# Optimization experiments

Hardware: AMD Instinct MI355X
Metric: run time of the kernel (lower is better)

The kernel has to match this reference:

```python
import jax, jax.numpy as jnp
import numpy as np

B, M, D = 512, 96, 512
H = 8            # num_heads
DH = D // H      # head dim
NC = 3           # num_clusters
BETA = 5
MEM = 1024       # memory_size
EPS = 1e-8


def _l2norm(x, axis=-1):
    # torch F.cosine_similarity clamps each norm at eps=1e-8
    n = jnp.linalg.norm(x, axis=axis, keepdims=True)
    return x / jnp.maximum(n, EPS)


def _dynamic_clustering(sims):
    # sims: (B, M). Sort descending, split into NC equal groups,
    # per-group mean and (unbiased) std. (dynamic_clustering is not
    # defined in the source repo; this is the assumed implementation.)
    s = -jnp.sort(-sims, axis=1)               # descending
    g = s.reshape(B, NC, M // NC)
    means = g.mean(axis=-1)                    # (B, NC)
    stds = jnp.std(g, axis=-1, ddof=1)         # (B, NC)
    return means, stds


def setup_inputs() -> dict:
    key = jax.random.key(0)
    ks = jax.random.split(key, 6)
    vis_global = jax.random.normal(ks[0], (B, D), dtype=jnp.float32)
    text_features = jax.random.normal(ks[1], (B, M, D), dtype=jnp.float32)
    scale = 1.0 / np.sqrt(D)
    in_proj_w = jax.random.normal(ks[2], (3 * D, D), dtype=jnp.float32) * scale
    in_proj_b = jnp.zeros((3 * D,), dtype=jnp.float32)
    out_proj_w = jax.random.normal(ks[3], (D, D), dtype=jnp.float32) * scale
    out_proj_b = jnp.zeros((D,), dtype=jnp.float32)
    text_memory = jax.random.normal(ks[4], (MEM, D), dtype=jnp.float32)
    tau_p_log = jnp.log(jnp.asarray(0.1, dtype=jnp.float32))
    tau_n_log = jnp.log(jnp.asarray(0.05, dtype=jnp.float32))
    return dict(vis_global=vis_global, text_features=text_features,
                in_proj_w=in_proj_w, in_proj_b=in_proj_b,
                out_proj_w=out_proj_w, out_proj_b=out_proj_b,
                text_memory=text_memory, tau_p_log=tau_p_log, tau_n_log=tau_n_log)


def reference(vis_global, text_features, in_proj_w, in_proj_b,
              out_proj_w, out_proj_b, text_memory, tau_p_log, tau_n_log):
    # --- dynamic clustering over visual-text cosine sims ---
    sims = jnp.einsum('bd,bmd->bm', _l2norm(vis_global), _l2norm(text_features))
    means, stds = _dynamic_clustering(sims)
    cluster_scores = means / (stds + 1e-6)     # (B, NC)

    # --- MultiheadAttention: 1-token query, M-token key/value ---
    wq, wk, wv = in_proj_w[:D], in_proj_w[D:2 * D], in_proj_w[2 * D:]
    bq, bk, bv = in_proj_b[:D], in_proj_b[D:2 * D], in_proj_b[2 * D:]
    q = (vis_global @ wq.T + bq).reshape(B, H, DH)              # (B,H,DH)
    k = (text_features @ wk.T + bk).reshape(B, M, H, DH)        # (B,M,H,DH)
    v = (text_features @ wv.T + bv).reshape(B, M, H, DH)
    attn = jax.nn.softmax(jnp.einsum('bhd,bmhd->bhm', q, k) / np.sqrt(DH), axis=-1)
    ctx = jnp.einsum('bhm,bmhd->bhd', attn, v).reshape(B, D)
    corrected = ctx @ out_proj_w.T + out_proj_b                 # (B, D)

    tau_p = jnp.exp(tau_p_log)
    tau_n = jnp.exp(tau_n_log)
    pos_sim = jnp.sum(_l2norm(vis_global) * _l2norm(corrected), axis=-1)  # (B,)

    # memory-bank scatter (ptr starts at 0) + negatives, all detached
    corr_sg = jax.lax.stop_gradient(corrected)
    mem = text_memory.at[0:B].set(corr_sg)
    all_negs = jnp.concatenate([jnp.roll(corr_sg, 1, axis=0), mem], axis=0)  # (B+MEM, D)

    neg_sims = _l2norm(vis_global) @ _l2norm(all_negs).T        # (B, B+MEM)
    hard_negs, _ = jax.lax.top_k(neg_sims, BETA)                # (B, BETA)

    pos_term = jnp.exp(pos_sim / tau_p)
    neg_terms = jnp.exp(hard_negs / tau_n).sum(axis=1)
    loss = -jnp.mean(jnp.log(pos_term / (pos_term + neg_terms + 1e-8)))
    return loss, corrected, cluster_scores
```

## Files before the change

kernel.cpp:

```cpp
#include <hip/hip_runtime.h>
#include <math.h>

typedef unsigned short u16;
typedef unsigned int u32;
typedef __attribute__((ext_vector_type(8))) short short8;
typedef __attribute__((ext_vector_type(4))) float f32x4;

#define EPS 1e-8f

__device__ inline float bf2f(u16 u) {
    union { u32 i; float f; } v; v.i = ((u32)u) << 16; return v.f;
}
__device__ inline u16 f2bf(float f) {
    union { float f; u32 u; } v; v.f = f;
    u32 r = v.u + 0x7fffu + ((v.u >> 16) & 1u);
    return (u16)(r >> 16);
}
__device__ inline u32 pack2(float a, float b) {
    return (u32)f2bf(a) | ((u32)f2bf(b) << 16);
}
__device__ inline float wave_sum(float v) {
    for (int off = 32; off; off >>= 1) v += __shfl_xor(v, off, 64);
    return v;
}

__global__ __launch_bounds__(256) void prep(const float* __restrict__ vis,
                                            const float* __restrict__ ipw,
                                            const float* __restrict__ opw,
                                            float* __restrict__ vis_n,
                                            u16* __restrict__ vis_nb,
                                            u16* __restrict__ vis_b,
                                            u16* __restrict__ wqb,
                                            u16* __restrict__ wvb,
                                            u16* __restrict__ wob,
                                            float* __restrict__ loss0)
{
    int bid = blockIdx.x;
    if (bid >= 128) {
        int i = ((bid - 128) * 256 + threadIdx.x) * 4;
        const float* src; u16* dst; int j;
        if (i < 262144)      { j = i;          src = ipw + j;          dst = wqb + j; }
        else if (i < 524288) { j = i - 262144; src = ipw + 524288 + j; dst = wvb + j; }
        else                 { j = i - 524288; src = opw + j;          dst = wob + j; }
        float4 v = *(const float4*)src;
        uint2 pk; pk.x = pack2(v.x, v.y); pk.y = pack2(v.z, v.w);
        *(uint2*)dst = pk;
        return;
    }
    if (bid == 0 && threadIdx.x == 0) loss0[0] = 0.0f;
    int wave = threadIdx.x >> 6, lane = threadIdx.x & 63;
    int b = bid * 4 + wave;
    const float* row = vis + b * 512 + lane * 8;
    float4 x0 = *(const float4*)row;
    float4 x1 = *(const float4*)(row + 4);
    uint4 rk;
    rk.x = pack2(x0.x, x0.y); rk.y = pack2(x0.z, x0.w);
    rk.z = pack2(x1.x, x1.y); rk.w = pack2(x1.z, x1.w);
    *(uint4*)(vis_b + b*512 + lane*8) = rk;
    float ss = x0.x*x0.x + x0.y*x0.y + x0.z*x0.z + x0.w*x0.w
             + x1.x*x1.x + x1.y*x1.y + x1.z*x1.z + x1.w*x1.w;
    ss = wave_sum(ss);
    float inv = 1.0f / fmaxf(sqrtf(ss), EPS);
    float4 y0, y1;
    y0.x = x0.x*inv; y0.y = x0.y*inv; y0.z = x0.z*inv; y0.w = x0.w*inv;
    y1.x = x1.x*inv; y1.y = x1.y*inv; y1.z = x1.z*inv; y1.w = x1.w*inv;
    *(float4*)(vis_n + b*512 + lane*8)     = y0;
    *(float4*)(vis_n + b*512 + lane*8 + 4) = y1;
    uint4 pk;
    pk.x = pack2(y0.x, y0.y); pk.y = pack2(y0.z, y0.w);
    pk.z = pack2(y1.x, y1.y); pk.w = pack2(y1.z, y1.w);
    *(uint4*)(vis_nb + b*512 + lane*8) = pk;
}

__global__ __launch_bounds__(256) void gemm64(const u16* __restrict__ A, int lda,
                                              const u16* __restrict__ B,
                                              const float* __restrict__ bias,
                                              float* __restrict__ Cf, int ldc)
{
    __shared__ __align__(16) u16 As[64 * 64];
    __shared__ __align__(16) u16 Bs[64 * 64];
    const int t = threadIdx.x, lane = t & 63, w = t >> 6;
    const int m0 = blockIdx.x * 64, n0 = blockIdx.y * 64;
    const int wm = (w >> 1) * 32, wn = (w & 1) * 32;
    const int l16 = lane & 15, quad = lane >> 4;
    const int srow = t >> 3, scol = (t & 7) * 8;

    f32x4 acc[2][2];
    for (int i = 0; i < 2; i++)
        for (int j = 0; j < 2; j++)
            for (int e = 0; e < 4; e++) acc[i][j][e] = 0.f;

    for (int ko = 0; ko < 512; ko += 64) {
        __syncthreads();
        #pragma unroll
        for (int i = 0; i < 2; i++) {
            int row = i * 32 + srow;
            *(uint4*)&As[row * 64 + scol] = *(const uint4*)&A[(size_t)(m0 + row) * lda + ko + scol];
            *(uint4*)&Bs[row * 64 + scol] = *(const uint4*)&B[(size_t)(n0 + row) * 512 + ko + scol];
        }
        __syncthreads();
        #pragma unroll
        for (int ks = 0; ks < 2; ks++) {
            short8 af[2], bfr[2];
            #pragma unroll
            for (int i = 0; i < 2; i++)
                af[i] = *(const short8*)&As[(wm + i * 16 + l16) * 64 + ks * 32 + quad * 8];
            #pragma unroll
            for (int j = 0; j < 2; j++)
                bfr[j] = *(const short8*)&Bs[(wn + j * 16 + l16) * 64 + ks * 32 + quad * 8];
            #pragma unroll
            for (int i = 0; i < 2; i++)
                #pragma unroll
                for (int j = 0; j < 2; j++)
                    acc[i][j] = __builtin_amdgcn_mfma_f32_16x16x32_bf16(af[i], bfr[j], acc[i][j], 0, 0, 0);
        }
    }
    for (int i = 0; i < 2; i++) {
        int row = m0 + wm + i * 16 + quad * 4;
        for (int j = 0; j < 2; j++) {
            int col = n0 + wn + j * 16 + l16;
            float bv = bias ? bias[col] : 0.f;
            for (int r = 0; r < 4; r++)
                Cf[(size_t)(row + r) * ldc + col] = acc[i][j][r] + bv;
        }
    }
}

__global__ __launch_bounds__(256) void gemm_head(const u16* __restrict__ u_allb,
                                                 const u16* __restrict__ wvb,
                                                 const float* __restrict__ bv,
                                                 u16* __restrict__ ctxb)
{
    const int h = blockIdx.y;
    const u16* A = u_allb + h * 512;
    const u16* B = wvb + (size_t)h * 64 * 512;
    __shared__ __align__(16) u16 As[64 * 64];
    __shared__ __align__(16) u16 Bs[64 * 64];
    const int t = threadIdx.x, lane = t & 63, w = t >> 6;
    const int m0 = blockIdx.x * 64;
    const int wm = (w >> 1) * 32, wn = (w & 1) * 32;
    const int l16 = lane & 15, quad = lane >> 4;
    const int srow = t >> 3, scol = (t & 7) * 8;

    f32x4 acc[2][2];
    for (int i = 0; i < 2; i++)
        for (int j = 0; j < 2; j++)
            for (int e = 0; e < 4; e++) acc[i][j][e] = 0.f;

    for (int ko = 0; ko < 512; ko += 64) {
        __syncthreads();
        #pragma unroll
        for (int i = 0; i < 2; i++) {
            int row = i * 32 + srow;
            *(uint4*)&As[row * 64 + scol] = *(const uint4*)&A[(size_t)(m0 + row) * 4096 + ko + scol];
            *(uint4*)&Bs[row * 64 + scol] = *(const uint4*)&B[(size_t)row * 512 + ko + scol];
        }
        __syncthreads();
        #pragma unroll
        for (int ks = 0; ks < 2; ks++) {
            short8 af[2], bfr[2];
            #pragma unroll
            for (int i = 0; i < 2; i++)
                af[i] = *(const short8*)&As[(wm + i * 16 + l16) * 64 + ks * 32 + quad * 8];
            #pragma unroll
            for (int j = 0; j < 2; j++)
                bfr[j] = *(const short8*)&Bs[(wn + j * 16 + l16) * 64 + ks * 32 + quad * 8];
            #pragma unroll
            for (int i = 0; i < 2; i++)
                #pragma unroll
                for (int j = 0; j < 2; j++)
                    acc[i][j] = __builtin_amdgcn_mfma_f32_16x16x32_bf16(af[i], bfr[j], acc[i][j], 0, 0, 0);
        }
    }
    for (int i = 0; i < 2; i++) {
        int row = m0 + wm + i * 16 + quad * 4;
        for (int j = 0; j < 2; j++) {
            int col = wn + j * 16 + l16;
            float bb = bv[h * 64 + col];
            for (int r = 0; r < 4; r++)
                ctxb[(size_t)(row + r) * 512 + h * 64 + col] = f2bf(acc[i][j][r] + bb);
        }
    }
}

__global__ __launch_bounds__(256) void qk_proj(const float* __restrict__ q,
                                               const float* __restrict__ wk,
                                               float* __restrict__ qk_all)
{
    int bg = blockIdx.x, h = blockIdx.y;
    int t = threadIdx.x;
    int j = blockIdx.z * 256 + t;
    __shared__ float q8[8][64];
    {
        int r = t >> 5;
        int d0 = (t & 31) * 2;
        const float* qp = q + (bg * 8 + r) * 512 + h * 64 + d0;
        q8[r][d0] = qp[0]; q8[r][d0 + 1] = qp[1];
    }
    __syncthreads();
    float acc[8] = {0, 0, 0, 0, 0, 0, 0, 0};
    const float* wrow = wk + (size_t)(h * 64) * 512 + j;
    #pragma unroll 4
    for (int d = 0; d < 64; d++) {
        float ww = wrow[(size_t)d * 512];
        #pragma unroll
        for (int r = 0; r < 8; r++) acc[r] += q8[r][d] * ww;
    }
    #pragma unroll
    for (int r = 0; r < 8; r++)
        qk_all[((size_t)(bg * 8 + r) * 8 + h) * 512 + j] = acc[r];
}

__global__ __launch_bounds__(1024) void fused_attn(const float* __restrict__ tf,
                                                   const float* __restrict__ vis_n,
                                                   const float* __restrict__ qk_all,
                                                   u16* __restrict__ u_allb,
                                                   float* __restrict__ out_cs)
{
    __shared__ __align__(16) u16 Xs[96 * 520];
    __shared__ __align__(16) u16 Qs[16 * 520];
    __shared__ __align__(16) u16 Ps[16 * 104];
    __shared__ float Sc[16 * 100];
    __shared__ float sm_[96], srt[96], linv[8];

    const int b = blockIdx.x;
    const int t = threadIdx.x, w = t >> 6, lane = t & 63;
    const int l16 = lane & 15, quad = lane >> 4;

    const float4* v4 = (const float4*)(vis_n + b * 512 + lane * 8);
    float4 va = v4[0], vb = v4[1];

    if (w < 8) {
        const float4* q4 = (const float4*)(qk_all + ((size_t)b * 8 + w) * 512 + lane * 8);
        float4 a = q4[0], c = q4[1];
        uint4 pk;
        pk.x = pack2(a.x, a.y); pk.y = pack2(a.z, a.w);
        pk.z = pack2(c.x, c.y); pk.w = pack2(c.z, c.w);
        *(uint4*)&Qs[w * 520 + lane * 8] = pk;
    }

    #pragma unroll
    for (int i = 0; i < 3; i++) {
        int m0r = w + i * 32;
        int m1r = m0r + 16;
        const float4* x4a = (const float4*)(tf + ((size_t)b * 96 + m0r) * 512 + lane * 8);
        const float4* x4b = (const float4*)(tf + ((size_t)b * 96 + m1r) * 512 + lane * 8);
        float4 a0 = x4a[0], c0 = x4a[1];
        float4 a1 = x4b[0], c1 = x4b[1];
        float ss0 = a0.x*a0.x + a0.y*a0.y + a0.z*a0.z + a0.w*a0.w
                  + c0.x*c0.x + c0.y*c0.y + c0.z*c0.z + c0.w*c0.w;
        float dt0 = a0.x*va.x + a0.y*va.y + a0.z*va.z + a0.w*va.w
                  + c0.x*vb.x + c0.y*vb.y + c0.z*vb.z + c0.w*vb.w;
        float ss1 = a1.x*a1.x + a1.y*a1.y + a1.z*a1.z + a1.w*a1.w
                  + c1.x*c1.x + c1.y*c1.y + c1.z*c1.z + c1.w*c1.w;
        float dt1 = a1.x*va.x + a1.y*va.y + a1.z*va.z + a1.w*va.w
                  + c1.x*vb.x + c1.y*vb.y + c1.z*vb.z + c1.w*vb.w;
        #pragma unroll
        for (int off = 32; off; off >>= 1) {
            ss0 += __shfl_xor(ss0, off, 64);
            dt0 += __shfl_xor(dt0, off, 64);
            ss1 += __shfl_xor(ss1, off, 64);
            dt1 += __shfl_xor(dt1, off, 64);
        }
        if (lane == 0) {
            sm_[m0r] = dt0 / fmaxf(sqrtf(ss0), EPS);
            sm_[m1r] = dt1 / fmaxf(sqrtf(ss1), EPS);
        }
        uint4 pk0, pk1;
        pk0.x = pack2(a0.x, a0.y); pk0.y = pack2(a0.z, a0.w);
        pk0.z = pack2(c0.x, c0.y); pk0.w = pack2(c0.z, c0.w);
        pk1.x = pack2(a1.x, a1.y); pk1.y = pack2(a1.z, a1.w);
        pk1.z = pack2(c1.x, c1.y); pk1.w = pack2(c1.z, c1.w);
        *(uint4*)&Xs[m0r * 520 + lane * 8] = pk0;
        *(uint4*)&Xs[m1r * 520 + lane * 8] = pk1;
    }
    __syncthreads();

    if (w < 6) {
        f32x4 acc;
        for (int e = 0; e < 4; e++) acc[e] = 0.f;
        #pragma unroll
        for (int ks = 0; ks < 16; ks++) {
            short8 a = *(const short8*)&Xs[(w * 16 + l16) * 520 + ks * 32 + quad * 8];
            short8 q = *(const short8*)&Qs[l16 * 520 + ks * 32 + quad * 8];
            acc = __builtin_amdgcn_mfma_f32_16x16x32_bf16(a, q, acc, 0, 0, 0);
        }
        #pragma unroll
        for (int r = 0; r < 4; r++)
            Sc[l16 * 100 + w * 16 + quad * 4 + r] = acc[r] * 0.125f;
    }
    __syncthreads();

    if (w < 8) {
        float e0 = __expf(Sc[w * 100 + lane]);
        float e1 = (lane < 32) ? __expf(Sc[w * 100 + 64 + lane]) : 0.f;
        float l = wave_sum(e0 + e1);
        Ps[w * 104 + lane] = f2bf(e0);
        if (lane < 32) Ps[w * 104 + 64 + lane] = f2bf(e1);
        if (lane == 0) linv[w] = 1.0f / l;
    }
    if (t < 96) {
        float v = sm_[t]; int r = 0;
        for (int j = 0; j < 96; j++) {
            float u = sm_[j];
            r += (u > v) || (u == v && j < t);
        }
        srt[r] = v;
    }
    __syncthreads();

    #pragma unroll
    for (int jj = 0; jj < 2; jj++) {
        int n0 = (w * 2 + jj) * 16;
        f32x4 acc;
        for (int e = 0; e < 4; e++) acc[e] = 0.f;
        #pragma unroll
        for (int ks = 0; ks < 3; ks++) {
            short8 ap = *(const short8*)&Ps[l16 * 104 + ks * 32 + quad * 8];
            short8 bx;
            #pragma unroll
            for (int j = 0; j < 8; j++)
                bx[j] = (short)Xs[(ks * 32 + quad * 8 + j) * 520 + n0 + l16];
            acc = __builtin_amdgcn_mfma_f32_16x16x32_bf16(ap, bx, acc, 0, 0, 0);
        }
        if (quad < 2) {
            #pragma unroll
            for (int r = 0; r < 4; r++) {
                int h = quad * 4 + r;
                u_allb[((size_t)b * 8 + h) * 512 + n0 + l16] = f2bf(acc[r] * linv[h]);
            }
        }
    }
    if (t < 3) {
        float mean = 0.f;
        #pragma unroll 8
        for (int i = 0; i < 32; i++) mean += srt[t * 32 + i];
        mean *= (1.0f / 32.0f);
        float var = 0.f;
        #pragma unroll 8
        for (int i = 0; i < 32; i++) { float d = srt[t * 32 + i] - mean; var += d * d; }
        var *= (1.0f / 31.0f);
        out_cs[b * 3 + t] = mean / (sqrtf(var) + 1e-6f);
    }
}

__global__ __launch_bounds__(256) void negs_build(const float* __restrict__ corrected,
                                                  const float* __restrict__ tm,
                                                  const float* __restrict__ vis_n,
                                                  u16* __restrict__ negs_nb,
                                                  float* __restrict__ pos)
{
    int wave = threadIdx.x >> 6, lane = threadIdx.x & 63;
    int j = blockIdx.x * 4 + wave;
    const float* src = (j < 512) ? (corrected + j * 512) : (tm + j * 512);
    const float* row = src + lane * 8;
    float4 x0 = *(const float4*)row;
    float4 x1 = *(const float4*)(row + 4);
    float ss = x0.x*x0.x + x0.y*x0.y + x0.z*x0.z + x0.w*x0.w
             + x1.x*x1.x + x1.y*x1.y + x1.z*x1.z + x1.w*x1.w;
    float dt = 0.f;
    if (j < 512) {
        const float* vn = vis_n + j * 512 + lane * 8;
        float4 v0 = *(const float4*)vn;
        float4 v1 = *(const float4*)(vn + 4);
        dt = x0.x*v0.x + x0.y*v0.y + x0.z*v0.z + x0.w*v0.w
           + x1.x*v1.x + x1.y*v1.y + x1.z*v1.z + x1.w*v1.w;
    }
    ss = wave_sum(ss);
    dt = wave_sum(dt);
    float inv = 1.0f / fmaxf(sqrtf(ss), EPS);
    float4 y0, y1;
    y0.x = x0.x*inv; y0.y = x0.y*inv; y0.z = x0.z*inv; y0.w = x0.w*inv;
    y1.x = x1.x*inv; y1.y = x1.y*inv; y1.z = x1.z*inv; y1.w = x1.w*inv;
    uint4 pk;
    pk.x = pack2(y0.x, y0.y); pk.y = pack2(y0.z, y0.w);
    pk.z = pack2(y1.x, y1.y); pk.w = pack2(y1.z, y1.w);
    *(uint4*)(negs_nb + j * 512 + lane * 8) = pk;
    if (j < 512 && lane == 0) pos[j] = dt * inv;
}

__global__ __launch_bounds__(256) void topk_loss(const float* __restrict__ ns,
                                                 const float* __restrict__ pos,
                                                 const float* __restrict__ tau_p_log,
                                                 const float* __restrict__ tau_n_log,
                                                 float* __restrict__ out_loss)
{
    int b = blockIdx.x, t = threadIdx.x;
    int w = t >> 6, lane = t & 63;
    __shared__ float cand_v[4];
    __shared__ int   cand_m[4];

    const float4 raw = *(const float4*)(ns + b * 1024 + t * 4);
    float lv[4] = {raw.x, raw.y, raw.z, raw.w};
    #pragma unroll
    for (int i = 1; i < 4; i++) {
        float key = lv[i];
        int j = i - 1;
        #pragma unroll
        for (int k = 0; k < 3; k++) {
            if (j >= 0 && lv[j] < key) { lv[j + 1] = lv[j]; j--; }
        }
        lv[j + 1] = key;
    }
    int lp = 0;

    float tn = expf(tau_n_log[0]);
    float inv_tn = 1.0f / tn;
    float nsum = 0.f;
    int collected = 0;

    for (int round = 0; round < 5 && collected < 5; round++) {
        float head = (lp < 4) ? lv[lp] : -1e30f;
        float mv = head; int ml = lane;
        #pragma unroll
        for (int off = 32; off; off >>= 1) {
            float ov = __shfl_xor(mv, off, 64);
            int   ol = __shfl_xor(ml, off, 64);
            if (ov > mv || (ov == mv && ol < ml)) { mv = ov; ml = ol; }
        }
        if (lane == 0) { cand_v[w] = mv; cand_m[w] = ml; }
        __syncthreads();
        float bv = cand_v[0]; int bw = 0;
        #pragma unroll
        for (int i = 1; i < 4; i++) {
            if (cand_v[i] > bv) { bv = cand_v[i]; bw = i; }
        }
        int bl = cand_m[bw];
        __syncthreads();
        if (w == bw && lane == bl) lp++;
        int wm = ((bw * 64 + bl) < 128) ? 2 : 1;
        int take = (wm < (5 - collected)) ? wm : (5 - collected);
        nsum += (float)take * __expf(bv * inv_tn);
        collected += take;
    }

    if (t == 0) {
        float tp = expf(tau_p_log[0]);
        float p = expf(pos[b] / tp);
        float term = logf(p / (p + nsum + 1e-8f));
        atomicAdd(out_loss, -term * (1.0f / 512.0f));
    }
}

extern "C" void kernel_launch(void* const* d_in, const int* in_sizes, int n_in,
                              void* d_out, int out_size, void* d_ws, size_t ws_size,
                              hipStream_t stream) {
    const float* vis = (const float*)d_in[0];
    const float* tf  = (const float*)d_in[1];
    const float* ipw = (const float*)d_in[2];
    const float* ipb = (const float*)d_in[3];
    const float* opw = (const float*)d_in[4];
    const float* opb = (const float*)d_in[5];
    const float* tm  = (const float*)d_in[6];
    const float* tpl = (const float*)d_in[7];
    const float* tnl = (const float*)d_in[8];

    float* out       = (float*)d_out;
    float* out_loss  = out;
    float* out_corr  = out + 1;
    float* out_cs    = out + 1 + 512 * 512;

    char* p = (char*)d_ws;
    auto alloc = [&](size_t bytes) { char* r = p; p += (bytes + 255) & ~(size_t)255; return r; };
    float* vis_n  = (float*)alloc(512 * 512 * 4);
    u16*   vis_nb = (u16*)  alloc(512 * 512 * 2);
    u16*   vis_b  = (u16*)  alloc(512 * 512 * 2);
    u16*   wqb    = (u16*)  alloc(512 * 512 * 2);
    u16*   wvb    = (u16*)  alloc(512 * 512 * 2);
    u16*   wob    = (u16*)  alloc(512 * 512 * 2);
    float* qws    = (float*)alloc(512 * 512 * 4);
    float* qk_all = (float*)alloc((size_t)512 * 8 * 512 * 4);
    u16*   u_allb = (u16*)  alloc((size_t)512 * 8 * 512 * 2);
    u16*   ctxb   = (u16*)  alloc(512 * 512 * 2);
    u16*   negsb  = (u16*)  alloc(1024 * 512 * 2);
    float* ns     = (float*)alloc(512 * 1024 * 4);
    float* pos    = (float*)alloc(512 * 4);

    const float* wk = ipw + 512 * 512;
    const float* bv = ipb + 2 * 512;

    prep<<<896, 256, 0, stream>>>(vis, ipw, opw, vis_n, vis_nb, vis_b, wqb, wvb, wob, out_loss);
    gemm64<<<dim3(8, 8), 256, 0, stream>>>(vis_b, 512, wqb, ipb, qws, 512);
    qk_proj<<<dim3(64, 8, 2), 256, 0, stream>>>(qws, wk, qk_all);
    fused_attn<<<512, 1024, 0, stream>>>(tf, vis_n, qk_all, u_allb, out_cs);
    gemm_head<<<dim3(8, 8), 256, 0, stream>>>(u_allb, wvb, bv, ctxb);
    gemm64<<<dim3(8, 8), 256, 0, stream>>>(ctxb, 512, wob, opb, out_corr, 512);
    negs_build<<<256, 256, 0, stream>>>(out_corr, tm, vis_n, negsb, pos);
    gemm64<<<dim3(8, 16), 256, 0, stream>>>(vis_nb, 512, negsb, nullptr, ns, 1024);
    topk_loss<<<512, 256, 0, stream>>>(ns, pos, tpl, tnl, out_loss);
}
```

Baseline: 244.2 us.

## Fuse prep, Q projection and QK projection into one kernel; convert weights on load

Replaces the prep kernel, the Q-projection GEMM and the qk_proj kernel with one fused_pre kernel. Its blocks normalize the visual rows, normalize the memory-bank negatives early, or compute Q per (batch-group, head) with MFMA and then multiply by a transposed Wk tile held in LDS. The separate bf16 weight-conversion pass is removed: gemm_head and the out-projection GEMM now convert fp32 weights to bf16 as they load them. The goal is fewer launches and fewer intermediate global round trips. In exchange, each QK block reloads Wk and transposes it with scattered LDS writes, using a large LDS footprint (~70KB) that may limit occupancy, and the downstream GEMMs re-read and re-convert fp32 weights.

```diff
diff --git a/kernel.cpp b/kernel.cpp
--- a/kernel.cpp
+++ b/kernel.cpp
@@ -24,56 +24,139 @@
     return v;
 }
 
-__global__ __launch_bounds__(256) void prep(const float* __restrict__ vis,
-                                            const float* __restrict__ ipw,
-                                            const float* __restrict__ opw,
-                                            float* __restrict__ vis_n,
-                                            u16* __restrict__ vis_nb,
-                                            u16* __restrict__ vis_b,
-                                            u16* __restrict__ wqb,
-                                            u16* __restrict__ wvb,
-                                            u16* __restrict__ wob,
-                                            float* __restrict__ loss0)
+__global__ __launch_bounds__(256) void fused_pre(const float* __restrict__ vis,
+                                                 const float* __restrict__ ipw,
+                                                 const float* __restrict__ ipb,
+                                                 const float* __restrict__ tm,
+                                                 float* __restrict__ vis_n,
+                                                 u16* __restrict__ vis_nb,
+                                                 u16* __restrict__ negsb,
+                                                 float* __restrict__ qk_all,
+                                                 float* __restrict__ loss0)
 {
-    int bid = blockIdx.x;
-    if (bid >= 128) {
-        int i = ((bid - 128) * 256 + threadIdx.x) * 4;
-        const float* src; u16* dst; int j;
-        if (i < 262144)      { j = i;          src = ipw + j;          dst = wqb + j; }
-        else if (i < 524288) { j = i - 262144; src = ipw + 524288 + j; dst = wvb + j; }
-        else                 { j = i - 524288; src = opw + j;          dst = wob + j; }
-        float4 v = *(const float4*)src;
-        uint2 pk; pk.x = pack2(v.x, v.y); pk.y = pack2(v.z, v.w);
-        *(uint2*)dst = pk;
+    __shared__ __align__(16) u16 BsT[512 * 66];
+    __shared__ __align__(16) u16 As[16 * 64];
+    __shared__ __align__(16) u16 Bs[64 * 64];
+    __shared__ __align__(16) u16 Qs[16 * 64];
+
+    const int bid = blockIdx.x;
+    const int t = threadIdx.x, w = t >> 6, lane = t & 63;
+
+    if (bid < 128) {
+        if (bid == 0 && t == 0) loss0[0] = 0.0f;
+        int b = bid * 4 + w;
+        const float* row = vis + b * 512 + lane * 8;
+        float4 x0 = *(const float4*)row;
+        float4 x1 = *(const float4*)(row + 4);
+        float ss = x0.x*x0.x + x0.y*x0.y + x0.z*x0.z + x0.w*x0.w
+                 + x1.x*x1.x + x1.y*x1.y + x1.z*x1.z + x1.w*x1.w;
+        ss = wave_sum(ss);
+        float inv = 1.0f / fmaxf(sqrtf(ss), EPS);
+        float4 y0, y1;
+        y0.x = x0.x*inv; y0.y = x0.y*inv; y0.z = x0.z*inv; y0.w = x0.w*inv;
+        y1.x = x1.x*inv; y1.y = x1.y*inv; y1.z = x1.z*inv; y1.w = x1.w*inv;
+        *(float4*)(vis_n + b*512 + lane*8)     = y0;
+        *(float4*)(vis_n + b*512 + lane*8 + 4) = y1;
+        uint4 pk;
+        pk.x = pack2(y0.x, y0.y); pk.y = pack2(y0.z, y0.w);
+        pk.z = pack2(y1.x, y1.y); pk.w = pack2(y1.z, y1.w);
+        *(uint4*)(vis_nb + b*512 + lane*8) = pk;
         return;
     }
-    if (bid == 0 && threadIdx.x == 0) loss0[0] = 0.0f;
-    int wave = threadIdx.x >> 6, lane = threadIdx.x & 63;
-    int b = bid * 4 + wave;
-    const float* row = vis + b * 512 + lane * 8;
-    float4 x0 = *(const float4*)row;
-    float4 x1 = *(const float4*)(row + 4);
-    uint4 rk;
-    rk.x = pack2(x0.x, x0.y); rk.y = pack2(x0.z, x0.w);
-    rk.z = pack2(x1.x, x1.y); rk.w = pack2(x1.z, x1.w);
-    *(uint4*)(vis_b + b*512 + lane*8) = rk;
-    float ss = x0.x*x0.x + x0.y*x0.y + x0.z*x0.z + x0.w*x0.w
-             + x1.x*x1.x + x1.y*x1.y + x1.z*x1.z + x1.w*x1.w;
-    ss = wave_sum(ss);
-    float inv = 1.0f / fmaxf(sqrtf(ss), EPS);
-    float4 y0, y1;
-    y0.x = x0.x*inv; y0.y = x0.y*inv; y0.z = x0.z*inv; y0.w = x0.w*inv;
-    y1.x = x1.x*inv; y1.y = x1.y*inv; y1.z = x1.z*inv; y1.w = x1.w*inv;
-    *(float4*)(vis_n + b*512 + lane*8)     = y0;
-    *(float4*)(vis_n + b*512 + lane*8 + 4) = y1;
-    uint4 pk;
-    pk.x = pack2(y0.x, y0.y); pk.y = pack2(y0.z, y0.w);
-    pk.z = pack2(y1.x, y1.y); pk.w = pack2(y1.z, y1.w);
-    *(uint4*)(vis_nb + b*512 + lane*8) = pk;
-}
-
+    if (bid >= 384) {
+        int j = 512 + (bid - 384) * 4 + w;
+        const float* row = tm + (size_t)j * 512 + lane * 8;
+        float4 x0 = *(const float4*)row;
+        float4 x1 = *(const float4*)(row + 4);
+        float ss = x0.x*x0.x + x0.y*x0.y + x0.z*x0.z + x0.w*x0.w
+                 + x1.x*x1.x + x1.y*x1.y + x1.z*x1.z + x1.w*x1.w;
+        ss = wave_sum(ss);
+        float inv = 1.0f / fmaxf(sqrtf(ss), EPS);
+        uint4 pk;
+        pk.x = pack2(x0.x*inv, x0.y*inv); pk.y = pack2(x0.z*inv, x0.w*inv);
+        pk.z = pack2(x1.x*inv, x1.y*inv); pk.w = pack2(x1.z*inv, x1.w*inv);
+        *(uint4*)(negsb + (size_t)j * 512 + lane * 8) = pk;
+        return;
+    }
+
+    const int idx = bid - 128;
+    const int bg = idx >> 3, h = idx & 7;
+    const int m0 = bg * 16;
+    const int l16 = lane & 15, quad = lane >> 4;
+
+    f32x4 acc;
+    for (int e = 0; e < 4; e++) acc[e] = 0.f;
+    const float* wqbase = ipw + (size_t)(h * 64) * 512;
+    for (int ko = 0; ko < 512; ko += 64) {
+        __syncthreads();
+        if (t < 128) {
+            int row = t >> 3, col = (t & 7) * 8;
+            const float* s = vis + (size_t)(m0 + row) * 512 + ko + col;
+            float4 a = *(const float4*)s, c = *(const float4*)(s + 4);
+            uint4 pk;
+            pk.x = pack2(a.x, a.y); pk.y = pack2(a.z, a.w);
+            pk.z = pack2(c.x, c.y); pk.w = pack2(c.z, c.w);
+            *(uint4*)&As[row * 64 + col] = pk;
+        }
+        #pragma unroll
+        for (int i = 0; i < 2; i++) {
+            int s = t + 256 * i;
+            int row = s >> 3, col = (s & 7) * 8;
+            const float* src = wqbase + (size_t)row * 512 + ko + col;
+            float4 a = *(const float4*)src, c = *(const float4*)(src + 4);
+            uint4 pk;
+            pk.x = pack2(a.x, a.y); pk.y = pack2(a.z, a.w);
+            pk.z = pack2(c.x, c.y); pk.w = pack2(c.z, c.w);
+            *(uint4*)&Bs[row * 64 + col] = pk;
+        }
+        __syncthreads();
+        #pragma unroll
+        for (int ks = 0; ks < 2; ks++) {
+            short8 af = *(const short8*)&As[l16 * 64 + ks * 32 + quad * 8];
+            short8 bf = *(const short8*)&Bs[(w * 16 + l16) * 64 + ks * 32 + quad * 8];
+            acc = __builtin_amdgcn_mfma_f32_16x16x32_bf16(af, bf, acc, 0, 0, 0);
+        }
+    }
+    {
+        float bq = ipb[h * 64 + w * 16 + l16];
+        #pragma unroll
+        for (int r = 0; r < 4; r++)
+            Qs[(quad * 4 + r) * 64 + w * 16 + l16] = f2bf(acc[r] + bq);
+    }
+    __syncthreads();
+    const float* wkbase = ipw + (size_t)(512 + h * 64) * 512;
+    #pragma unroll
+    for (int i = 0; i < 32; i++) {
+        int s = t + 256 * i;
+        int d = s >> 7;
+        int jc = (s & 127) * 4;
+        float4 a = *(const float4*)(wkbase + (size_t)d * 512 + jc);
+        BsT[(jc + 0) * 66 + d] = f2bf(a.x);
+        BsT[(jc + 1) * 66 + d] = f2bf(a.y);
+        BsT[(jc + 2) * 66 + d] = f2bf(a.z);
+        BsT[(jc + 3) * 66 + d] = f2bf(a.w);
+    }
+    __syncthreads();
+    #pragma unroll
+    for (int i = 0; i < 8; i++) {
+        int n0 = (i * 4 + w) * 16;
+        f32x4 a2;
+        for (int e = 0; e < 4; e++) a2[e] = 0.f;
+        #pragma unroll
+        for (int ks = 0; ks < 2; ks++) {
+            short8 af = *(const short8*)&Qs[l16 * 64 + ks * 32 + quad * 8];
+            short8 bf = *(const short8*)&BsT[(n0 + l16) * 66 + ks * 32 + quad * 8];
+            a2 = __builtin_amdgcn_mfma_f32_16x16x32_bf16(af, bf, a2, 0, 0, 0);
+        }
+        #pragma unroll
+        for (int r = 0; r < 4; r++)
+            qk_all[((size_t)(m0 + quad * 4 + r) * 8 + h) * 512 + n0 + l16] = a2[r];
+    }
+}
+
+template<bool BF32>
 __global__ __launch_bounds__(256) void gemm64(const u16* __restrict__ A, int lda,
-                                              const u16* __restrict__ B,
+                                              const void* __restrict__ Bv,
                                               const float* __restrict__ bias,
                                               float* __restrict__ Cf, int ldc)
 {
@@ -96,7 +179,16 @@
         for (int i = 0; i < 2; i++) {
             int row = i * 32 + srow;
             *(uint4*)&As[row * 64 + scol] = *(const uint4*)&A[(size_t)(m0 + row) * lda + ko + scol];
-            *(uint4*)&Bs[row * 64 + scol] = *(const uint4*)&B[(size_t)(n0 + row) * 512 + ko + scol];
+            if (BF32) {
+                const float* src = (const float*)Bv + (size_t)(n0 + row) * 512 + ko + scol;
+                float4 a = *(const float4*)src, c = *(const float4*)(src + 4);
+                uint4 pk;
+                pk.x = pack2(a.x, a.y); pk.y = pack2(a.z, a.w);
+                pk.z = pack2(c.x, c.y); pk.w = pack2(c.z, c.w);
+                *(uint4*)&Bs[row * 64 + scol] = pk;
+            } else {
+                *(uint4*)&Bs[row * 64 + scol] = *(const uint4*)&((const u16*)Bv)[(size_t)(n0 + row) * 512 + ko + scol];
+            }
         }
         __syncthreads();
         #pragma unroll
@@ -127,13 +219,13 @@
 }
 
 __global__ __launch_bounds__(256) void gemm_head(const u16* __restrict__ u_allb,
-                                                 const u16* __restrict__ wvb,
+                                                 const float* __restrict__ wv,
                                                  const float* __restrict__ bv,
                                                  u16* __restrict__ ctxb)
 {
     const int h = blockIdx.y;
     const u16* A = u_allb + h * 512;
-    const u16* B = wvb + (size_t)h * 64 * 512;
+    const float* B = wv + (size_t)h * 64 * 512;
     __shared__ __align__(16) u16 As[64 * 64];
     __shared__ __align__(16) u16 Bs[64 * 64];
     const int t = threadIdx.x, lane = t & 63, w = t >> 6;
@@ -153,7 +245,12 @@
         for (int i = 0; i < 2; i++) {
             int row = i * 32 + srow;
             *(uint4*)&As[row * 64 + scol] = *(const uint4*)&A[(size_t)(m0 + row) * 4096 + ko + scol];
-            *(uint4*)&Bs[row * 64 + scol] = *(const uint4*)&B[(size_t)row * 512 + ko + scol];
+            const float* src = B + (size_t)row * 512 + ko + scol;
+            float4 a = *(const float4*)src, c = *(const float4*)(src + 4);
+            uint4 pk;
+            pk.x = pack2(a.x, a.y); pk.y = pack2(a.z, a.w);
+            pk.z = pack2(c.x, c.y); pk.w = pack2(c.z, c.w);
+            *(uint4*)&Bs[row * 64 + scol] = pk;
         }
         __syncthreads();
         #pragma unroll
@@ -181,34 +278,6 @@
                 ctxb[(size_t)(row + r) * 512 + h * 64 + col] = f2bf(acc[i][j][r] + bb);
         }
     }
-}
-
-__global__ __launch_bounds__(256) void qk_proj(const float* __restrict__ q,
-                                               const float* __restrict__ wk,
-                                               float* __restrict__ qk_all)
-{
-    int bg = blockIdx.x, h = blockIdx.y;
-    int t = threadIdx.x;
-    int j = blockIdx.z * 256 + t;
-    __shared__ float q8[8][64];
-    {
-        int r = t >> 5;
-        int d0 = (t & 31) * 2;
-        const float* qp = q + (bg * 8 + r) * 512 + h * 64 + d0;
-        q8[r][d0] = qp[0]; q8[r][d0 + 1] = qp[1];
-    }
-    __syncthreads();
-    float acc[8] = {0, 0, 0, 0, 0, 0, 0, 0};
-    const float* wrow = wk + (size_t)(h * 64) * 512 + j;
-    #pragma unroll 4
-    for (int d = 0; d < 64; d++) {
-        float ww = wrow[(size_t)d * 512];
-        #pragma unroll
-        for (int r = 0; r < 8; r++) acc[r] += q8[r][d] * ww;
-    }
-    #pragma unroll
-    for (int r = 0; r < 8; r++)
-        qk_all[((size_t)(bg * 8 + r) * 8 + h) * 512 + j] = acc[r];
 }
 
 __global__ __launch_bounds__(1024) void fused_attn(const float* __restrict__ tf,
@@ -344,39 +413,31 @@
     }
 }
 
-__global__ __launch_bounds__(256) void negs_build(const float* __restrict__ corrected,
-                                                  const float* __restrict__ tm,
-                                                  const float* __restrict__ vis_n,
-                                                  u16* __restrict__ negs_nb,
-                                                  float* __restrict__ pos)
+__global__ __launch_bounds__(256) void negs_corr(const float* __restrict__ corrected,
+                                                 const float* __restrict__ vis_n,
+                                                 u16* __restrict__ negs_nb,
+                                                 float* __restrict__ pos)
 {
     int wave = threadIdx.x >> 6, lane = threadIdx.x & 63;
     int j = blockIdx.x * 4 + wave;
-    const float* src = (j < 512) ? (corrected + j * 512) : (tm + j * 512);
-    const float* row = src + lane * 8;
+    const float* row = corrected + (size_t)j * 512 + lane * 8;
     float4 x0 = *(const float4*)row;
     float4 x1 = *(const float4*)(row + 4);
     float ss = x0.x*x0.x + x0.y*x0.y + x0.z*x0.z + x0.w*x0.w
              + x1.x*x1.x + x1.y*x1.y + x1.z*x1.z + x1.w*x1.w;
-    float dt = 0.f;
-    if (j < 512) {
-        const float* vn = vis_n + j * 512 + lane * 8;
-        float4 v0 = *(const float4*)vn;
-        float4 v1 = *(const float4*)(vn + 4);
-        dt = x0.x*v0.x + x0.y*v0.y + x0.z*v0.z + x0.w*v0.w
-           + x1.x*v1.x + x1.y*v1.y + x1.z*v1.z + x1.w*v1.w;
-    }
+    const float* vn = vis_n + j * 512 + lane * 8;
+    float4 v0 = *(const float4*)vn;
+    float4 v1 = *(const float4*)(vn + 4);
+    float dt = x0.x*v0.x + x0.y*v0.y + x0.z*v0.z + x0.w*v0.w
+             + x1.x*v1.x + x1.y*v1.y + x1.z*v1.z + x1.w*v1.w;
     ss = wave_sum(ss);
     dt = wave_sum(dt);
     float inv = 1.0f / fmaxf(sqrtf(ss), EPS);
-    float4 y0, y1;
-    y0.x = x0.x*inv; y0.y = x0.y*inv; y0.z = x0.z*inv; y0.w = x0.w*inv;
-    y1.x = x1.x*inv; y1.y = x1.y*inv; y1.z = x1.z*inv; y1.w = x1.w*inv;
     uint4 pk;
-    pk.x = pack2(y0.x, y0.y); pk.y = pack2(y0.z, y0.w);
-    pk.z = pack2(y1.x, y1.y); pk.w = pack2(y1.z, y1.w);
-    *(uint4*)(negs_nb + j * 512 + lane * 8) = pk;
-    if (j < 512 && lane == 0) pos[j] = dt * inv;
+    pk.x = pack2(x0.x*inv, x0.y*inv); pk.y = pack2(x0.z*inv, x0.w*inv);
+    pk.z = pack2(x1.x*inv, x1.y*inv); pk.w = pack2(x1.z*inv, x1.w*inv);
+    *(uint4*)(negs_nb + (size_t)j * 512 + lane * 8) = pk;
+    if (lane == 0) pos[j] = dt * inv;
 }
 
 __global__ __launch_bounds__(256) void topk_loss(const float* __restrict__ ns,
@@ -464,11 +525,6 @@
     auto alloc = [&](size_t bytes) { char* r = p; p += (bytes + 255) & ~(size_t)255; return r; };
     float* vis_n  = (float*)alloc(512 * 512 * 4);
     u16*   vis_nb = (u16*)  alloc(512 * 512 * 2);
-    u16*   vis_b  = (u16*)  alloc(512 * 512 * 2);
-    u16*   wqb    = (u16*)  alloc(512 * 512 * 2);
-    u16*   wvb    = (u16*)  alloc(512 * 512 * 2);
-    u16*   wob    = (u16*)  alloc(512 * 512 * 2);
-    float* qws    = (float*)alloc(512 * 512 * 4);
     float* qk_all = (float*)alloc((size_t)512 * 8 * 512 * 4);
     u16*   u_allb = (u16*)  alloc((size_t)512 * 8 * 512 * 2);
     u16*   ctxb   = (u16*)  alloc(512 * 512 * 2);
@@ -476,16 +532,14 @@
     float* ns     = (float*)alloc(512 * 1024 * 4);
     float* pos    = (float*)alloc(512 * 4);
 
-    const float* wk = ipw + 512 * 512;
+    const float* wv = ipw + 2 * 512 * 512;
     const float* bv = ipb + 2 * 512;
 
-    prep<<<896, 256, 0, stream>>>(vis, ipw, opw, vis_n, vis_nb, vis_b, wqb, wvb, wob, out_loss);
-    gemm64<<<dim3(8, 8), 256, 0, stream>>>(vis_b, 512, wqb, ipb, qws, 512);
-    qk_proj<<<dim3(64, 8, 2), 256, 0, stream>>>(qws, wk, qk_all);
+    fused_pre<<<512, 256, 0, stream>>>(vis, ipw, ipb, tm, vis_n, vis_nb, negsb, qk_all, out_loss);
     fused_attn<<<512, 1024, 0, stream>>>(tf, vis_n, qk_all, u_allb, out_cs);
-    gemm_head<<<dim3(8, 8), 256, 0, stream>>>(u_allb, wvb, bv, ctxb);
-    gemm64<<<dim3(8, 8), 256, 0, stream>>>(ctxb, 512, wob, opb, out_corr, 512);
-    negs_build<<<256, 256, 0, stream>>>(out_corr, tm, vis_n, negsb, pos);
-    gemm64<<<dim3(8, 16), 256, 0, stream>>>(vis_nb, 512, negsb, nullptr, ns, 1024);
+    gemm_head<<<dim3(8, 8), 256, 0, stream>>>(u_allb, wv, bv, ctxb);
+    gemm64<true><<<dim3(8, 8), 256, 0, stream>>>(ctxb, 512, opw, opb, out_corr, 512);
+    negs_corr<<<128, 256, 0, stream>>>(out_corr, vis_n, negsb, pos);
+    gemm64<false><<<dim3(8, 16), 256, 0, stream>>>(vis_nb, 512, negsb, nullptr, ns, 1024);
     topk_loss<<<512, 256, 0, stream>>>(ns, pos, tpl, tnl, out_loss);
 }
```

New measurement: 254.3 us. 4.1% more time.
